# Kernel optimization log

Measured on AMD Instinct MI355X. Metric: run time of the kernel, lower is better.

The kernel has to match this reference:

```python
import jax, jax.numpy as jnp
import numpy as np

N_NODES = 100000
N_EDGES = 1600000
IN_DIM, H1, H2, N_CLASSES = 128, 64, 64, 16
NEG_SLOPE = 0.2  # PyG GATConv default leaky_relu slope


def _xavier(key, shape, gain=1.414):
    fan_in, fan_out = shape[0], shape[-1]
    a = gain * np.sqrt(6.0 / (fan_in + fan_out))
    return jax.random.uniform(key, shape, jnp.float32, -a, a)


def setup_inputs() -> dict:
    key = jax.random.key(0)
    ks = jax.random.split(key, 12)
    ft_list = jax.random.normal(ks[0], (N_NODES, IN_DIM), jnp.float32)
    adj_tensor = jax.random.randint(ks[1], (2, N_EDGES), 0, N_NODES, jnp.int64)
    return {
        "ft_list": ft_list,
        "adj_tensor": adj_tensor,
        "W1": _xavier(ks[2], (IN_DIM, H1)),
        "a_src1": _xavier(ks[3], (H1, 1))[:, 0],
        "a_dst1": _xavier(ks[4], (H1, 1))[:, 0],
        "b1": jnp.zeros((H1,), jnp.float32),
        "W2": _xavier(ks[5], (H1, H2)),
        "a_src2": _xavier(ks[6], (H2, 1))[:, 0],
        "a_dst2": _xavier(ks[7], (H2, 1))[:, 0],
        "b2": jnp.zeros((H2,), jnp.float32),
        "clas_W": _xavier(ks[8], (H2, N_CLASSES)),
        "clas_b": _xavier(ks[9], (1, N_CLASSES)),
    }


def _gat_conv(x, src, dst, n, W, a_src, a_dst, b):
    # h: [N, H] transformed node features
    h = x @ W
    alpha_s = h @ a_src  # [N]
    alpha_d = h @ a_dst  # [N]
    # per-edge attention logit (gather)
    e = jax.nn.leaky_relu(alpha_s[src] + alpha_d[dst], NEG_SLOPE)  # [E]
    # segment softmax over edges grouped by destination node
    m = jax.ops.segment_max(e, dst, num_segments=n)
    p = jnp.exp(e - m[dst])
    s = jax.ops.segment_sum(p, dst, num_segments=n)
    attn = p / s[dst]  # [E]
    # weighted scatter-add of source features
    out = jax.ops.segment_sum(h[src] * attn[:, None], dst, num_segments=n)
    return out + b


def reference(ft_list, adj_tensor, W1, a_src1, a_dst1, b1, W2, a_src2, a_dst2, b2, clas_W, clas_b):
    n = ft_list.shape[0]
    loop = jnp.arange(n, dtype=adj_tensor.dtype)
    src = jnp.concatenate([adj_tensor[0], loop])  # add self-loops (PyG default)
    dst = jnp.concatenate([adj_tensor[1], loop])
    x = _gat_conv(ft_list, src, dst, n, W1, a_src1, a_dst1, b1)
    x = jax.nn.elu(x)
    # dropout(0.5) is identity in eval mode
    x = _gat_conv(x, src, dst, n, W2, a_src2, a_dst2, b2)
    logits = x @ clas_W + clas_b
    return logits, x
```

## Files before the change

### kernel.cpp

```cpp
#include <hip/hip_runtime.h>
#include <hip/hip_bf16.h>

#define NEG_SLOPE 0.2f
#define BSH 9
#define BW  (1 << BSH)
#define CH  4096
#define PGRID 256

typedef short short8 __attribute__((ext_vector_type(8)));
typedef float f32x4 __attribute__((ext_vector_type(4)));


__global__ __launch_bounds__(256) void bucket_hist_kernel(
    const int* __restrict__ adj, int* __restrict__ H, int E, int N, int R, int NBK)
{
    __shared__ int hist[256];
    const int t = threadIdx.x;
    const int ET = E + N;
    for (int r = blockIdx.x; r < R; r += gridDim.x) {
        hist[t] = 0;
        __syncthreads();
        int base = r * CH;
        for (int i = 0; i < CH / 256; ++i) {
            int e = base + i * 256 + t;
            if (e >= ET) break;
            int d = (e < E) ? adj[E + e] : (e - E);
            atomicAdd(&hist[d >> BSH], 1);
        }
        __syncthreads();
        if (t < NBK) H[r * NBK + t] = hist[t];
        __syncthreads();
    }
}

__global__ __launch_bounds__(256) void scan_rounds_kernel(
    const int* __restrict__ H, int* __restrict__ S2, int* __restrict__ tot,
    int R, int NBK)
{
    __shared__ int part[256];
    const int b = blockIdx.x;
    const int t = threadIdx.x;
    const int C = (R + 255) / 256;
    int r0 = t * C, r1 = min(R, r0 + C);
    int s = 0;
    for (int r = r0; r < r1; ++r) s += H[r * NBK + b];
    part[t] = s;
    __syncthreads();
    for (int off = 1; off < 256; off <<= 1) {
        int v = (t >= off) ? part[t - off] : 0;
        __syncthreads();
        part[t] += v;
        __syncthreads();
    }
    int run = (t > 0) ? part[t - 1] : 0;
    for (int r = r0; r < r1; ++r) {
        int h = H[r * NBK + b];
        S2[r * NBK + b] = run;
        run += h;
    }
    if (t == 255) tot[b] = part[255];
}

__global__ __launch_bounds__(256) void scan_tot_kernel(
    const int* __restrict__ tot, int* __restrict__ base, int NBK)
{
    __shared__ int s[256];
    int t = threadIdx.x;
    int v = (t < NBK) ? tot[t] : 0;
    s[t] = v;
    __syncthreads();
    for (int off = 1; off < 256; off <<= 1) {
        int u = (t >= off) ? s[t - off] : 0;
        __syncthreads();
        s[t] += u;
        __syncthreads();
    }
    if (t < NBK) base[t] = s[t] - v;
}

__global__ __launch_bounds__(256) void partition_kernel(
    const int* __restrict__ adj, const int* __restrict__ S2,
    const int* __restrict__ base, int* __restrict__ pbuf,
    int E, int N, int R, int NBK)
{
    __shared__ int lcur[256];
    const int t = threadIdx.x;
    const int ET = E + N;
    for (int r = blockIdx.x; r < R; r += gridDim.x) {
        if (t < NBK) lcur[t] = base[t] + S2[r * NBK + t];
        __syncthreads();
        int b0 = r * CH;
        for (int i = 0; i < CH / 256; ++i) {
            int e = b0 + i * 256 + t;
            if (e >= ET) break;
            int s, d;
            if (e < E) { d = adj[E + e]; s = adj[e]; }
            else       { s = d = e - E; }
            int b = d >> BSH;
            int pos = atomicAdd(&lcur[b], 1);
            pbuf[pos] = (s << BSH) | (d & (BW - 1));
        }
        __syncthreads();
    }
}

__global__ __launch_bounds__(256) void csr_build_kernel(
    const int* __restrict__ base, const int* __restrict__ tot,
    const int* __restrict__ pbuf,
    int* __restrict__ row_ptr, int* __restrict__ col_idx, int E, int N, int NBK)
{
    __shared__ int offA[BW];
    __shared__ int lcur[BW];
    const int b = blockIdx.x;
    const int t = threadIdx.x;
    const int node0 = b << BSH;
    const int nn = min(BW, N - node0);
    const int ET = E + N;
    const int segbeg = base[b];
    const int segend = segbeg + tot[b];

    offA[t] = 0; offA[t + 256] = 0;
    __syncthreads();
    for (int i = segbeg + t; i < segend; i += 256)
        atomicAdd(&offA[pbuf[i] & (BW - 1)], 1);
    __syncthreads();
    for (int off = 1; off < BW; off <<= 1) {
        int i1 = t + 256;
        int v0 = (t >= off) ? offA[t - off] : 0;
        int v1 = (i1 >= off) ? offA[i1 - off] : 0;
        __syncthreads();
        offA[t] += v0; offA[i1] += v1;
        __syncthreads();
    }
    if (t < nn) {
        int ex = t ? offA[t - 1] : 0;
        row_ptr[node0 + t] = segbeg + ex;
        lcur[t] = segbeg + ex;
    }
    int i2 = t + 256;
    if (i2 < nn) {
        int ex = offA[i2 - 1];
        row_ptr[node0 + i2] = segbeg + ex;
        lcur[i2] = segbeg + ex;
    }
    if (b == NBK - 1 && t == 0) row_ptr[N] = ET;
    __syncthreads();
    for (int i = segbeg + t; i < segend; i += 256) {
        int p = pbuf[i];
        int pos = atomicAdd(&lcur[p & (BW - 1)], 1);
        col_idx[pos] = p >> BSH;
    }
}


__device__ __forceinline__ float bf_to_f(unsigned short u)
{
    return __uint_as_float((unsigned)u << 16);
}

__device__ __forceinline__ unsigned short f2bf(float f)
{
    union { __hip_bfloat16 b; unsigned short u; } v;
    v.b = __float2bfloat16(f);
    return v.u;
}

__global__ __launch_bounds__(256) void prep_wfrag_kernel(
    const float* __restrict__ W, unsigned short* __restrict__ wf, int K)
{
    int total = K * 64;
    int idx = blockIdx.x * 256 + threadIdx.x;
    if (idx >= total) return;
    int i = idx & 7;
    int l = (idx >> 3) & 63;
    int f = idx >> 9;
    int s = f >> 2, tt = f & 3;
    int k = 32 * s + 8 * (l >> 4) + i;
    int n = 16 * tt + (l & 15);
    wf[idx] = f2bf(W[k * 64 + n]);
}

template<int K>
__global__ __launch_bounds__(256) void gemm_alpha_mfma(
    const float* __restrict__ X, const unsigned short* __restrict__ wf,
    const float* __restrict__ a_src, const float* __restrict__ a_dst,
    __hip_bfloat16* __restrict__ h, float* __restrict__ as_, float* __restrict__ ad_,
    int N, int nChunks)
{
    constexpr int S = K / 32;
    const int t = threadIdx.x;
    const int wave = t >> 6, lane = t & 63;
    const int g = lane >> 4, c = lane & 15;

    short8 bf[S * 4];
#pragma unroll
    for (int f = 0; f < S * 4; ++f)
        bf[f] = *(const short8*)(wf + ((size_t)(f * 64 + lane)) * 8);

    float asr[4], adr[4];
#pragma unroll
    for (int tt = 0; tt < 4; ++tt) {
        asr[tt] = a_src[16 * tt + c];
        adr[tt] = a_dst[16 * tt + c];
    }

    for (int chunk = blockIdx.x; chunk < nChunks; chunk += gridDim.x) {
        const int r0 = chunk * 64 + wave * 16;
        const int arow = r0 + c;
        const bool rv = arow < N;
        const float* xr = X + (size_t)arow * K;

        f32x4 acc[4];
#pragma unroll
        for (int tt = 0; tt < 4; ++tt) acc[tt] = (f32x4){0.f, 0.f, 0.f, 0.f};

#pragma unroll
        for (int s = 0; s < S; ++s) {
            float4 x0 = make_float4(0.f, 0.f, 0.f, 0.f);
            float4 x1 = make_float4(0.f, 0.f, 0.f, 0.f);
            if (rv) {
                const float4* p = (const float4*)(xr + 32 * s + 8 * g);
                x0 = p[0]; x1 = p[1];
            }
            float xs[8] = {x0.x, x0.y, x0.z, x0.w, x1.x, x1.y, x1.z, x1.w};
            union { short8 v; unsigned u[4]; } ah, al;
#pragma unroll
            for (int p2 = 0; p2 < 4; ++p2) {
                unsigned u0 = __float_as_uint(xs[2 * p2]);
                unsigned u1 = __float_as_uint(xs[2 * p2 + 1]);
                ah.u[p2] = (u0 >> 16) | (u1 & 0xffff0000u);
                float h0 = __uint_as_float(u0 & 0xffff0000u);
                float h1 = __uint_as_float(u1 & 0xffff0000u);
                unsigned l0 = __float_as_uint(xs[2 * p2] - h0);
                unsigned l1 = __float_as_uint(xs[2 * p2 + 1] - h1);
                al.u[p2] = (l0 >> 16) | (l1 & 0xffff0000u);
            }
#pragma unroll
            for (int tt = 0; tt < 4; ++tt) {
                acc[tt] = __builtin_amdgcn_mfma_f32_16x16x32_bf16(
                    ah.v, bf[s * 4 + tt], acc[tt], 0, 0, 0);
                acc[tt] = __builtin_amdgcn_mfma_f32_16x16x32_bf16(
                    al.v, bf[s * 4 + tt], acc[tt], 0, 0, 0);
            }
        }

#pragma unroll
        for (int i = 0; i < 4; ++i) {
            const int ri = r0 + 4 * g + i;
            float va = 0.f, vd = 0.f;
#pragma unroll
            for (int tt = 0; tt < 4; ++tt) {
                float v = acc[tt][i];
                va += v * asr[tt];
                vd += v * adr[tt];
                if (ri < N) h[(size_t)ri * 64 + 16 * tt + c] = __float2bfloat16(v);
            }
#pragma unroll
            for (int off = 8; off >= 1; off >>= 1) {
                va += __shfl_xor(va, off, 16);
                vd += __shfl_xor(vd, off, 16);
            }
            if (c == 0 && ri < N) { as_[ri] = va; ad_[ri] = vd; }
        }
    }
}

__global__ __launch_bounds__(256) void gat_aggregate_kernel(
    const int* __restrict__ row_ptr, const int* __restrict__ col_idx,
    const float* __restrict__ as_, const float* __restrict__ ad_,
    const __hip_bfloat16* __restrict__ h, const float* __restrict__ b,
    float* __restrict__ out, int N, int do_elu)
{
    int node = blockIdx.x * 4 + (threadIdx.x >> 6);
    int lane = threadIdx.x & 63;
    int sub = lane >> 4, q = lane & 15;
    if (node >= N) return;
    int beg = row_ptr[node], end = row_ptr[node + 1];
    float ad = ad_[node];
    float4 acc = make_float4(0.f, 0.f, 0.f, 0.f);
    float psum = 0.f;
    const ushort4* hb = (const ushort4*)h;
    for (int i = beg; i < end; i += 16) {
        int e0 = i + sub, e1 = i + 4 + sub, e2 = i + 8 + sub, e3 = i + 12 + sub;
        bool v0 = e0 < end, v1 = e1 < end, v2 = e2 < end, v3 = e3 < end;
        int s0 = col_idx[v0 ? e0 : end - 1];
        int s1 = col_idx[v1 ? e1 : end - 1];
        int s2 = col_idx[v2 ? e2 : end - 1];
        int s3 = col_idx[v3 ? e3 : end - 1];
        float x0 = as_[s0] + ad, x1 = as_[s1] + ad;
        float x2 = as_[s2] + ad, x3 = as_[s3] + ad;
        ushort4 u0 = hb[(size_t)s0 * 16 + q];
        ushort4 u1 = hb[(size_t)s1 * 16 + q];
        ushort4 u2 = hb[(size_t)s2 * 16 + q];
        ushort4 u3 = hb[(size_t)s3 * 16 + q];
        x0 = x0 > 0.f ? x0 : NEG_SLOPE * x0;
        x1 = x1 > 0.f ? x1 : NEG_SLOPE * x1;
        x2 = x2 > 0.f ? x2 : NEG_SLOPE * x2;
        x3 = x3 > 0.f ? x3 : NEG_SLOPE * x3;
        float p0 = v0 ? __expf(x0) : 0.f;
        float p1 = v1 ? __expf(x1) : 0.f;
        float p2 = v2 ? __expf(x2) : 0.f;
        float p3 = v3 ? __expf(x3) : 0.f;
        psum += (p0 + p1) + (p2 + p3);
        acc.x += p0 * bf_to_f(u0.x) + p1 * bf_to_f(u1.x) + p2 * bf_to_f(u2.x) + p3 * bf_to_f(u3.x);
        acc.y += p0 * bf_to_f(u0.y) + p1 * bf_to_f(u1.y) + p2 * bf_to_f(u2.y) + p3 * bf_to_f(u3.y);
        acc.z += p0 * bf_to_f(u0.z) + p1 * bf_to_f(u1.z) + p2 * bf_to_f(u2.z) + p3 * bf_to_f(u3.z);
        acc.w += p0 * bf_to_f(u0.w) + p1 * bf_to_f(u1.w) + p2 * bf_to_f(u2.w) + p3 * bf_to_f(u3.w);
    }
#pragma unroll
    for (int off = 16; off <= 32; off <<= 1) {
        acc.x += __shfl_xor(acc.x, off, 64);
        acc.y += __shfl_xor(acc.y, off, 64);
        acc.z += __shfl_xor(acc.z, off, 64);
        acc.w += __shfl_xor(acc.w, off, 64);
        psum  += __shfl_xor(psum,  off, 64);
    }
    if (sub == 0) {
        float inv = 1.f / psum;
        float4 bb = ((const float4*)b)[q];
        float4 v;
        v.x = acc.x * inv + bb.x;
        v.y = acc.y * inv + bb.y;
        v.z = acc.z * inv + bb.z;
        v.w = acc.w * inv + bb.w;
        if (do_elu) {
            v.x = v.x > 0.f ? v.x : (__expf(v.x) - 1.f);
            v.y = v.y > 0.f ? v.y : (__expf(v.y) - 1.f);
            v.z = v.z > 0.f ? v.z : (__expf(v.z) - 1.f);
            v.w = v.w > 0.f ? v.w : (__expf(v.w) - 1.f);
        }
        ((float4*)(out + (size_t)node * 64))[q] = v;
    }
}

__global__ __launch_bounds__(256) void classifier_kernel(
    const float* __restrict__ x, const float* __restrict__ cw,
    const float* __restrict__ cb, float* __restrict__ out, int N)
{
    int i = blockIdx.x * blockDim.x + threadIdx.x;
    if (i >= N * 16) return;
    int n = i >> 4, c = i & 15;
    const float4* xr = (const float4*)(x + (size_t)n * 64);
    float acc = cb[c];
#pragma unroll
    for (int j4 = 0; j4 < 16; ++j4) {
        float4 xv = xr[j4];
        acc += xv.x * cw[(j4 * 4 + 0) * 16 + c];
        acc += xv.y * cw[(j4 * 4 + 1) * 16 + c];
        acc += xv.z * cw[(j4 * 4 + 2) * 16 + c];
        acc += xv.w * cw[(j4 * 4 + 3) * 16 + c];
    }
    out[i] = acc;
}

extern "C" void kernel_launch(void* const* d_in, const int* in_sizes, int n_in,
                              void* d_out, int out_size, void* d_ws, size_t ws_size,
                              hipStream_t stream)
{
    const float* X    = (const float*)d_in[0];
    const int*   adj  = (const int*)d_in[1];
    const float* W1   = (const float*)d_in[2];
    const float* a_s1 = (const float*)d_in[3];
    const float* a_d1 = (const float*)d_in[4];
    const float* b1   = (const float*)d_in[5];
    const float* W2   = (const float*)d_in[6];
    const float* a_s2 = (const float*)d_in[7];
    const float* a_d2 = (const float*)d_in[8];
    const float* b2   = (const float*)d_in[9];
    const float* cW   = (const float*)d_in[10];
    const float* cb   = (const float*)d_in[11];

    const int N   = in_sizes[0] / 128;
    const int E   = in_sizes[1] / 2;
    const int ET  = E + N;
    const int R   = (ET + CH - 1) / CH;
    const int NBK = (N + BW - 1) >> BSH;

    __hip_bfloat16* A = (__hip_bfloat16*)d_ws;
    float* B       = (float*)(A + (size_t)N * 64);
    float* asb     = B + (size_t)N * 64;
    float* adb     = asb + N;
    int*   row_ptr = (int*)(adb + N);
    int*   col_idx = row_ptr + (N + 1);
    int*   pbuf    = col_idx + ET;
    int*   H       = pbuf + ET;
    int*   S2      = H + R * NBK;
    int*   tot     = S2 + R * NBK;
    int*   base    = tot + NBK;

    uintptr_t wp = ((uintptr_t)pbuf + 15) & ~(uintptr_t)15;
    unsigned short* wf1 = (unsigned short*)wp;
    unsigned short* wf2 = wf1 + 128 * 64;

    const int T = 256;
    const int aggBlocks  = (N + 3) / 4;
    const int nChunks    = (N + 63) / 64;
    const int gemmBlocks = nChunks < 512 ? nChunks : 512;

    bucket_hist_kernel<<<PGRID, T, 0, stream>>>(adj, H, E, N, R, NBK);
    scan_rounds_kernel<<<NBK, T, 0, stream>>>(H, S2, tot, R, NBK);
    scan_tot_kernel<<<1, T, 0, stream>>>(tot, base, NBK);
    partition_kernel<<<PGRID, T, 0, stream>>>(adj, S2, base, pbuf, E, N, R, NBK);
    csr_build_kernel<<<NBK, T, 0, stream>>>(base, tot, pbuf, row_ptr, col_idx, E, N, NBK);

    prep_wfrag_kernel<<<(128 * 64 + 255) / 256, T, 0, stream>>>(W1, wf1, 128);
    prep_wfrag_kernel<<<(64 * 64 + 255) / 256, T, 0, stream>>>(W2, wf2, 64);

    gemm_alpha_mfma<128><<<gemmBlocks, T, 0, stream>>>(
        X, wf1, a_s1, a_d1, A, asb, adb, N, nChunks);
    gat_aggregate_kernel<<<aggBlocks, T, 0, stream>>>(
        row_ptr, col_idx, asb, adb, A, b1, B, N, 1);

    float* out  = (float*)d_out;
    float* xout = out + (size_t)N * 16;
    gemm_alpha_mfma<64><<<gemmBlocks, T, 0, stream>>>(
        B, wf2, a_s2, a_d2, A, asb, adb, N, nChunks);
    gat_aggregate_kernel<<<aggBlocks, T, 0, stream>>>(
        row_ptr, col_idx, asb, adb, A, b2, xout, N, 0);

    classifier_kernel<<<(N * 16 + T - 1) / T, T, 0, stream>>>(
        xout, cW, cb, out, N);
}
```

Before: 321.4 us.

## Widen aggregate gathers to 16-byte loads and fold log2e into attention scores

The aggregation kernel now assigns 8 lanes per edge, each loading 16 bytes (8 bf16 values), so each wave handles 8 edges at once instead of 4. The main loop processes two edges per lane with no bounds predicates, followed by a masked tail loop. The attention scalars are pre-scaled by log2e in the transform kernel so the kernel can call hardware exp2, and leaky relu becomes fmaxf. Unsigned 32-bit byte offsets replace 64-bit indexing, and a wider shuffle reduction over more accumulators is added to cut gather instructions and address math.

```diff
diff --git a/kernel.cpp b/kernel.cpp
--- a/kernel.cpp
+++ b/kernel.cpp
@@ -2,6 +2,7 @@
 #include <hip/hip_bf16.h>
 
 #define NEG_SLOPE 0.2f
+#define LOG2E 1.4426950408889634f
 #define BSH 9
 #define BW  (1 << BSH)
 #define CH  4096
@@ -153,11 +154,6 @@
 }
 
 
-__device__ __forceinline__ float bf_to_f(unsigned short u)
-{
-    return __uint_as_float((unsigned)u << 16);
-}
-
 __device__ __forceinline__ unsigned short f2bf(float f)
 {
     union { __hip_bfloat16 b; unsigned short u; } v;
@@ -260,7 +256,7 @@
                 va += __shfl_xor(va, off, 16);
                 vd += __shfl_xor(vd, off, 16);
             }
-            if (c == 0 && ri < N) { as_[ri] = va; ad_[ri] = vd; }
+            if (c == 0 && ri < N) { as_[ri] = va * LOG2E; ad_[ri] = vd * LOG2E; }
         }
     }
 }
@@ -273,63 +269,82 @@
 {
     int node = blockIdx.x * 4 + (threadIdx.x >> 6);
     int lane = threadIdx.x & 63;
-    int sub = lane >> 4, q = lane & 15;
+    int sub = lane >> 3, q = lane & 7;
     if (node >= N) return;
     int beg = row_ptr[node], end = row_ptr[node + 1];
     float ad = ad_[node];
-    float4 acc = make_float4(0.f, 0.f, 0.f, 0.f);
+    float acc[8] = {0.f, 0.f, 0.f, 0.f, 0.f, 0.f, 0.f, 0.f};
     float psum = 0.f;
-    const ushort4* hb = (const ushort4*)h;
-    for (int i = beg; i < end; i += 16) {
-        int e0 = i + sub, e1 = i + 4 + sub, e2 = i + 8 + sub, e3 = i + 12 + sub;
-        bool v0 = e0 < end, v1 = e1 < end, v2 = e2 < end, v3 = e3 < end;
-        int s0 = col_idx[v0 ? e0 : end - 1];
-        int s1 = col_idx[v1 ? e1 : end - 1];
-        int s2 = col_idx[v2 ? e2 : end - 1];
-        int s3 = col_idx[v3 ? e3 : end - 1];
-        float x0 = as_[s0] + ad, x1 = as_[s1] + ad;
-        float x2 = as_[s2] + ad, x3 = as_[s3] + ad;
-        ushort4 u0 = hb[(size_t)s0 * 16 + q];
-        ushort4 u1 = hb[(size_t)s1 * 16 + q];
-        ushort4 u2 = hb[(size_t)s2 * 16 + q];
-        ushort4 u3 = hb[(size_t)s3 * 16 + q];
-        x0 = x0 > 0.f ? x0 : NEG_SLOPE * x0;
-        x1 = x1 > 0.f ? x1 : NEG_SLOPE * x1;
-        x2 = x2 > 0.f ? x2 : NEG_SLOPE * x2;
-        x3 = x3 > 0.f ? x3 : NEG_SLOPE * x3;
-        float p0 = v0 ? __expf(x0) : 0.f;
-        float p1 = v1 ? __expf(x1) : 0.f;
-        float p2 = v2 ? __expf(x2) : 0.f;
-        float p3 = v3 ? __expf(x3) : 0.f;
-        psum += (p0 + p1) + (p2 + p3);
-        acc.x += p0 * bf_to_f(u0.x) + p1 * bf_to_f(u1.x) + p2 * bf_to_f(u2.x) + p3 * bf_to_f(u3.x);
-        acc.y += p0 * bf_to_f(u0.y) + p1 * bf_to_f(u1.y) + p2 * bf_to_f(u2.y) + p3 * bf_to_f(u3.y);
-        acc.z += p0 * bf_to_f(u0.z) + p1 * bf_to_f(u1.z) + p2 * bf_to_f(u2.z) + p3 * bf_to_f(u3.z);
-        acc.w += p0 * bf_to_f(u0.w) + p1 * bf_to_f(u1.w) + p2 * bf_to_f(u2.w) + p3 * bf_to_f(u3.w);
-    }
-#pragma unroll
-    for (int off = 16; off <= 32; off <<= 1) {
-        acc.x += __shfl_xor(acc.x, off, 64);
-        acc.y += __shfl_xor(acc.y, off, 64);
-        acc.z += __shfl_xor(acc.z, off, 64);
-        acc.w += __shfl_xor(acc.w, off, 64);
-        psum  += __shfl_xor(psum,  off, 64);
+
+    const char* cbp = (const char*)col_idx;
+    const char* abp = (const char*)as_;
+    const char* hbp = (const char*)h;
+    const unsigned qb = (unsigned)q * 16u;
+
+    int base = beg;
+    unsigned co = (unsigned)(beg + sub) * 4u;
+    for (; base + 16 <= end; base += 16, co += 64u) {
+        int s0 = *(const int*)(cbp + co);
+        int s1 = *(const int*)(cbp + (co + 32u));
+        float x0 = *(const float*)(abp + ((unsigned)s0 << 2)) + ad;
+        float x1 = *(const float*)(abp + ((unsigned)s1 << 2)) + ad;
+        uint4 u0 = *(const uint4*)(hbp + (((unsigned)s0 << 7) + qb));
+        uint4 u1 = *(const uint4*)(hbp + (((unsigned)s1 << 7) + qb));
+        x0 = fmaxf(x0, NEG_SLOPE * x0);
+        x1 = fmaxf(x1, NEG_SLOPE * x1);
+        float p0 = __builtin_amdgcn_exp2f(x0);
+        float p1 = __builtin_amdgcn_exp2f(x1);
+        psum += p0 + p1;
+        unsigned w;
+        w = u0.x; acc[0] += p0 * __uint_as_float(w << 16); acc[1] += p0 * __uint_as_float(w & 0xffff0000u);
+        w = u0.y; acc[2] += p0 * __uint_as_float(w << 16); acc[3] += p0 * __uint_as_float(w & 0xffff0000u);
+        w = u0.z; acc[4] += p0 * __uint_as_float(w << 16); acc[5] += p0 * __uint_as_float(w & 0xffff0000u);
+        w = u0.w; acc[6] += p0 * __uint_as_float(w << 16); acc[7] += p0 * __uint_as_float(w & 0xffff0000u);
+        w = u1.x; acc[0] += p1 * __uint_as_float(w << 16); acc[1] += p1 * __uint_as_float(w & 0xffff0000u);
+        w = u1.y; acc[2] += p1 * __uint_as_float(w << 16); acc[3] += p1 * __uint_as_float(w & 0xffff0000u);
+        w = u1.z; acc[4] += p1 * __uint_as_float(w << 16); acc[5] += p1 * __uint_as_float(w & 0xffff0000u);
+        w = u1.w; acc[6] += p1 * __uint_as_float(w << 16); acc[7] += p1 * __uint_as_float(w & 0xffff0000u);
+    }
+    for (; base < end; base += 8, co += 32u) {
+        int e0 = base + sub;
+        bool v0 = e0 < end;
+        unsigned c0 = (unsigned)(v0 ? e0 : end - 1) * 4u;
+        int s0 = *(const int*)(cbp + c0);
+        float x0 = *(const float*)(abp + ((unsigned)s0 << 2)) + ad;
+        uint4 u0 = *(const uint4*)(hbp + (((unsigned)s0 << 7) + qb));
+        x0 = fmaxf(x0, NEG_SLOPE * x0);
+        float p0 = v0 ? __builtin_amdgcn_exp2f(x0) : 0.f;
+        psum += p0;
+        unsigned w;
+        w = u0.x; acc[0] += p0 * __uint_as_float(w << 16); acc[1] += p0 * __uint_as_float(w & 0xffff0000u);
+        w = u0.y; acc[2] += p0 * __uint_as_float(w << 16); acc[3] += p0 * __uint_as_float(w & 0xffff0000u);
+        w = u0.z; acc[4] += p0 * __uint_as_float(w << 16); acc[5] += p0 * __uint_as_float(w & 0xffff0000u);
+        w = u0.w; acc[6] += p0 * __uint_as_float(w << 16); acc[7] += p0 * __uint_as_float(w & 0xffff0000u);
+    }
+#pragma unroll
+    for (int off = 8; off <= 32; off <<= 1) {
+        psum += __shfl_xor(psum, off, 64);
+#pragma unroll
+        for (int j = 0; j < 8; ++j) acc[j] += __shfl_xor(acc[j], off, 64);
     }
     if (sub == 0) {
         float inv = 1.f / psum;
-        float4 bb = ((const float4*)b)[q];
-        float4 v;
-        v.x = acc.x * inv + bb.x;
-        v.y = acc.y * inv + bb.y;
-        v.z = acc.z * inv + bb.z;
-        v.w = acc.w * inv + bb.w;
+        const float* bq = b + q * 8;
+        float4 b0 = *(const float4*)bq;
+        float4 b1 = *(const float4*)(bq + 4);
+        float v[8];
+        v[0] = acc[0] * inv + b0.x; v[1] = acc[1] * inv + b0.y;
+        v[2] = acc[2] * inv + b0.z; v[3] = acc[3] * inv + b0.w;
+        v[4] = acc[4] * inv + b1.x; v[5] = acc[5] * inv + b1.y;
+        v[6] = acc[6] * inv + b1.z; v[7] = acc[7] * inv + b1.w;
         if (do_elu) {
-            v.x = v.x > 0.f ? v.x : (__expf(v.x) - 1.f);
-            v.y = v.y > 0.f ? v.y : (__expf(v.y) - 1.f);
-            v.z = v.z > 0.f ? v.z : (__expf(v.z) - 1.f);
-            v.w = v.w > 0.f ? v.w : (__expf(v.w) - 1.f);
+#pragma unroll
+            for (int j = 0; j < 8; ++j)
+                v[j] = v[j] > 0.f ? v[j] : (__expf(v[j]) - 1.f);
         }
-        ((float4*)(out + (size_t)node * 64))[q] = v;
+        float* op = out + (size_t)node * 64 + q * 8;
+        ((float4*)op)[0] = make_float4(v[0], v[1], v[2], v[3]);
+        ((float4*)op)[1] = make_float4(v[4], v[5], v[6], v[7]);
     }
 }
 
```

Result: faster. 312.3 us (-2.8%).
